# Performance work log

Measured on AMD Instinct MI355X. Metric: run time of the kernel, lower is better.

## Reference

```python
import jax, jax.numpy as jnp
import numpy as np

N_IN = 100000   # active voxels at coarse level
N_OUT = 400000  # active voxels at fine level
K = 8           # 2x2x2 kernel offsets of the inverse conv
P = 100000      # rulebook pairs per kernel offset
C_IN, C_OUT, C_SKIP = 128, 64, 64
EPS = 1e-5


def setup_inputs() -> dict:
    key = jax.random.key(0)
    k1, k2, k3, k4, k5, k6 = jax.random.split(key, 6)
    x_feats = jax.random.normal(k1, (N_IN, C_IN), jnp.float32)
    skip_feats = jax.random.normal(k2, (N_OUT, C_SKIP), jnp.float32)
    W_deconv = jax.random.normal(k3, (K, C_IN, C_OUT), jnp.float32) * (1.0 / np.sqrt(C_IN * K))
    gamma = jnp.ones((C_OUT,), jnp.float32)
    beta = jnp.zeros((C_OUT,), jnp.float32)
    W_fuse = jax.random.normal(k4, (C_OUT + C_SKIP, C_OUT), jnp.float32) * (1.0 / np.sqrt(C_OUT + C_SKIP))
    in_idx = jax.random.randint(k5, (K, P), 0, N_IN, jnp.int32)
    out_idx = jax.random.randint(k6, (K, P), 0, N_OUT, jnp.int32)
    return {"x_feats": x_feats, "skip_feats": skip_feats, "W_deconv": W_deconv,
            "gamma": gamma, "beta": beta, "W_fuse": W_fuse,
            "in_idx": in_idx, "out_idx": out_idx}


def reference(x_feats, skip_feats, W_deconv, gamma, beta, W_fuse, in_idx, out_idx):
    # --- SparseInverseConv3d: gather-GEMM-scatter over the rulebook ---
    gathered = x_feats[in_idx]                                  # [K,P,C_IN]
    contrib = jnp.einsum('kpi,kio->kpo', gathered, W_deconv)    # [K,P,C_OUT]
    y = jnp.zeros((N_OUT, C_OUT), x_feats.dtype)
    y = y.at[out_idx.reshape(-1)].add(contrib.reshape(-1, C_OUT))
    # --- BatchNorm1d (batch stats, biased var) + ReLU on voxel features ---
    mean = jnp.mean(y, axis=0)
    var = jnp.mean((y - mean) ** 2, axis=0)
    y = (y - mean) * jax.lax.rsqrt(var + EPS) * gamma + beta
    y = jax.nn.relu(y)
    # --- channel concat with skip, then SubMConv3d(kernel=1) == linear ---
    z = jnp.concatenate([y, skip_feats], axis=1)                # [N_OUT, C_OUT+C_SKIP]
    return z @ W_fuse                                           # [N_OUT, C_OUT]
```

## Files before the change

kernel.cpp:

```cpp
#include <hip/hip_runtime.h>

#define N_IN   100000
#define N_OUT  400000
#define KK     8
#define PP     100000
#define C_IN   128
#define C_OUTC 64
#define C_SKIP 64
#define EPS_BN 1e-5f
#define SLOTS  16

typedef __attribute__((ext_vector_type(8))) short bf16x8;
typedef __attribute__((ext_vector_type(4))) float f32x4;

__device__ __forceinline__ unsigned short f2b(float f) {
    unsigned int u = __builtin_bit_cast(unsigned int, f);
    return (unsigned short)((u + 0x7FFFu + ((u >> 16) & 1u)) >> 16);
}
__device__ __forceinline__ float b2f(unsigned short v) {
    return __builtin_bit_cast(float, (unsigned)v << 16);
}

__global__ __launch_bounds__(256) void prep_all(
    const float4* __restrict__ x, const float* __restrict__ Wd,
    unsigned short* __restrict__ xb, unsigned short* __restrict__ bfrag,
    int4* __restrict__ counts4)
{
    const int t = blockIdx.x * 256 + threadIdx.x;
    if (t < N_IN * C_IN / 8) {
        const float4 v0 = x[2 * t], v1 = x[2 * t + 1];
        uint4 o;
        o.x = f2b(v0.x) | ((unsigned)f2b(v0.y) << 16);
        o.y = f2b(v0.z) | ((unsigned)f2b(v0.w) << 16);
        o.z = f2b(v1.x) | ((unsigned)f2b(v1.y) << 16);
        o.w = f2b(v1.z) | ((unsigned)f2b(v1.w) << 16);
        ((uint4*)xb)[t] = o;
    }
    if (t < N_OUT / 4)
        counts4[t] = (int4){0, 0, 0, 0};
    if (t < KK * 4 * 4 * 64 * 8) {
        const int j  = t & 7;
        const int l  = (t >> 3) & 63;
        const int ct = (t >> 9) & 3;
        const int ks = (t >> 11) & 3;
        const int ko = t >> 13;
        const int i  = ks * 32 + (l >> 4) * 8 + j;
        const int c  = ct * 16 + (l & 15);
        bfrag[t] = f2b(Wd[((size_t)ko * C_IN + i) * C_OUTC + c]);
    }
}

__global__ __launch_bounds__(256) void fill_csr(
    const int* __restrict__ in_idx, const int* __restrict__ out_idx,
    int* __restrict__ counts, int* __restrict__ slots)
{
    const int q = blockIdx.x * 256 + threadIdx.x;
    if (q < KK * PP) {
        const int row = out_idx[q];
        const int pk  = in_idx[q] * KK + q / PP;
        const int idx = atomicAdd(&counts[row], 1);
        if (idx < SLOTS) slots[(size_t)row * SLOTS + idx] = pk;
    }
}

__global__ __launch_bounds__(256) void gemm_all(
    const unsigned short* __restrict__ xb, const unsigned short* __restrict__ bfrag,
    unsigned short* __restrict__ z)
{
    __shared__ __align__(16) unsigned short alds[32 * 136];
    const int rb = blockIdx.x * 32;
    for (int cch = threadIdx.x; cch < 32 * 16; cch += 256) {
        const int row = cch >> 4, ch = cch & 15;
        *(uint4*)(&alds[row * 136 + ch * 8]) =
            *(const uint4*)(xb + (size_t)(rb + row) * C_IN + ch * 8);
    }
    __syncthreads();

    const int wv  = threadIdx.x >> 6;
    const int l   = threadIdx.x & 63;
    const int r16 = l & 15, hi = l >> 4;

    f32x4 acc[2][2][4];
    #pragma unroll
    for (int q = 0; q < 2; ++q)
        #pragma unroll
        for (int rt = 0; rt < 2; ++rt)
            #pragma unroll
            for (int ct = 0; ct < 4; ++ct)
                acc[q][rt][ct] = (f32x4){0.f, 0.f, 0.f, 0.f};

    #pragma unroll
    for (int ks = 0; ks < 4; ++ks) {
        const bf16x8 a0 = *(const bf16x8*)(&alds[r16 * 136 + ks * 32 + hi * 8]);
        const bf16x8 a1 = *(const bf16x8*)(&alds[(16 + r16) * 136 + ks * 32 + hi * 8]);
        #pragma unroll
        for (int q = 0; q < 2; ++q) {
            const unsigned short* __restrict__ bk = bfrag + (size_t)(wv * 2 + q) * 8192;
            #pragma unroll
            for (int ct = 0; ct < 4; ++ct) {
                const bf16x8 b = *(const bf16x8*)(bk + ((ks * 4 + ct) * 64 + l) * 8);
                acc[q][0][ct] = __builtin_amdgcn_mfma_f32_16x16x32_bf16(a0, b, acc[q][0][ct], 0, 0, 0);
                acc[q][1][ct] = __builtin_amdgcn_mfma_f32_16x16x32_bf16(a1, b, acc[q][1][ct], 0, 0, 0);
            }
        }
    }

    #pragma unroll
    for (int q = 0; q < 2; ++q) {
        const int k = wv * 2 + q;
        #pragma unroll
        for (int rt = 0; rt < 2; ++rt)
            #pragma unroll
            for (int ct = 0; ct < 4; ++ct)
                #pragma unroll
                for (int j = 0; j < 4; ++j)
                    z[((size_t)(rb + rt * 16 + hi * 4 + j) * KK + k) * 64 + ct * 16 + r16]
                        = f2b(acc[q][rt][ct][j]);
    }
}

__global__ __launch_bounds__(256) void gather_yb(
    const unsigned short* __restrict__ z, const int* __restrict__ counts,
    const int* __restrict__ slots, unsigned short* __restrict__ yb,
    float* __restrict__ partials)
{
    const int tid = threadIdx.x, lane = tid & 63;
    const int gw  = blockIdx.x * 4 + (tid >> 6);
    const int nw  = gridDim.x * 4;
    float ssum = 0.f, ssq = 0.f;

    for (int r0 = gw * 8; r0 < N_OUT; r0 += nw * 8) {
        const int4 c0 = *(const int4*)(counts + r0);
        const int4 c1 = *(const int4*)(counts + r0 + 4);
        const int cnt[8] = {c0.x, c0.y, c0.z, c0.w, c1.x, c1.y, c1.z, c1.w};
        int4 s4[8];
        #pragma unroll
        for (int i = 0; i < 8; ++i)
            s4[i] = *(const int4*)(slots + (size_t)(r0 + i) * SLOTS);

        float a[8];
        #pragma unroll
        for (int i = 0; i < 8; ++i) {
            const int c  = cnt[i] > SLOTS ? SLOTS : cnt[i];
            const int p0 = c > 0 ? s4[i].x : 0;
            const int p1 = c > 1 ? s4[i].y : 0;
            const int p2 = c > 2 ? s4[i].z : 0;
            const int p3 = c > 3 ? s4[i].w : 0;
            const float v0 = b2f(z[(size_t)p0 * 64 + lane]);
            const float v1 = b2f(z[(size_t)p1 * 64 + lane]);
            const float v2 = b2f(z[(size_t)p2 * 64 + lane]);
            const float v3 = b2f(z[(size_t)p3 * 64 + lane]);
            float s = (c > 0 ? v0 : 0.f) + (c > 1 ? v1 : 0.f);
            s += (c > 2 ? v2 : 0.f) + (c > 3 ? v3 : 0.f);
            if (c > 4) {
                for (int j = 4; j < c; ++j)
                    s += b2f(z[(size_t)slots[(size_t)(r0 + i) * SLOTS + j] * 64 + lane]);
            }
            a[i] = s;
        }
        #pragma unroll
        for (int i = 0; i < 8; ++i) {
            yb[(size_t)(r0 + i) * C_OUTC + lane] = f2b(a[i]);
            ssum += a[i];
            ssq = fmaf(a[i], a[i], ssq);
        }
    }

    __shared__ float rs[256], rq[256];
    rs[tid] = ssum; rq[tid] = ssq;
    __syncthreads();
    if (tid < 64) {
        const float s  = rs[tid] + rs[tid + 64] + rs[tid + 128] + rs[tid + 192];
        const float q2 = rq[tid] + rq[tid + 64] + rq[tid + 128] + rq[tid + 192];
        partials[(size_t)blockIdx.x * 128 + tid]      = s;
        partials[(size_t)blockIdx.x * 128 + 64 + tid] = q2;
    }
}

__global__ __launch_bounds__(256) void gather_y(
    const unsigned short* __restrict__ z, const int* __restrict__ counts,
    const int* __restrict__ slots, float* __restrict__ y,
    float* __restrict__ partials)
{
    const int tid = threadIdx.x, lane = tid & 63;
    const int gw  = blockIdx.x * 4 + (tid >> 6);
    const int nw  = gridDim.x * 4;
    float ssum = 0.f, ssq = 0.f;

    for (int r0 = gw * 8; r0 < N_OUT; r0 += nw * 8) {
        const int4 c0 = *(const int4*)(counts + r0);
        const int4 c1 = *(const int4*)(counts + r0 + 4);
        const int cnt[8] = {c0.x, c0.y, c0.z, c0.w, c1.x, c1.y, c1.z, c1.w};
        int4 s4[8];
        #pragma unroll
        for (int i = 0; i < 8; ++i)
            s4[i] = *(const int4*)(slots + (size_t)(r0 + i) * SLOTS);

        float a[8];
        #pragma unroll
        for (int i = 0; i < 8; ++i) {
            const int c  = cnt[i] > SLOTS ? SLOTS : cnt[i];
            const int p0 = c > 0 ? s4[i].x : 0;
            const int p1 = c > 1 ? s4[i].y : 0;
            const int p2 = c > 2 ? s4[i].z : 0;
            const int p3 = c > 3 ? s4[i].w : 0;
            const float v0 = b2f(z[(size_t)p0 * 64 + lane]);
            const float v1 = b2f(z[(size_t)p1 * 64 + lane]);
            const float v2 = b2f(z[(size_t)p2 * 64 + lane]);
            const float v3 = b2f(z[(size_t)p3 * 64 + lane]);
            float s = (c > 0 ? v0 : 0.f) + (c > 1 ? v1 : 0.f);
            s += (c > 2 ? v2 : 0.f) + (c > 3 ? v3 : 0.f);
            if (c > 4) {
                for (int j = 4; j < c; ++j)
                    s += b2f(z[(size_t)slots[(size_t)(r0 + i) * SLOTS + j] * 64 + lane]);
            }
            a[i] = s;
        }
        #pragma unroll
        for (int i = 0; i < 8; ++i) {
            y[(size_t)(r0 + i) * C_OUTC + lane] = a[i];
            ssum += a[i];
            ssq = fmaf(a[i], a[i], ssq);
        }
    }

    __shared__ float rs[256], rq[256];
    rs[tid] = ssum; rq[tid] = ssq;
    __syncthreads();
    if (tid < 64) {
        const float s  = rs[tid] + rs[tid + 64] + rs[tid + 128] + rs[tid + 192];
        const float q2 = rq[tid] + rq[tid + 64] + rq[tid + 128] + rq[tid + 192];
        partials[(size_t)blockIdx.x * 128 + tid]      = s;
        partials[(size_t)blockIdx.x * 128 + 64 + tid] = q2;
    }
}

__global__ __launch_bounds__(256) void reduce_mid(
    const float* __restrict__ partials, float* __restrict__ mid)
{
    const int col = threadIdx.x & 127, half = threadIdx.x >> 7;
    const int b   = blockIdx.x;
    float s = 0.f;
    #pragma unroll 4
    for (int r = half; r < 64; r += 2)
        s += partials[(size_t)(b * 64 + r) * 128 + col];
    __shared__ float sh[256];
    sh[threadIdx.x] = s;
    __syncthreads();
    if (half == 0) mid[(size_t)b * 128 + col] = s + sh[128 + col];
}

__global__ void finalize_p(const float* __restrict__ mid,
                           const float* __restrict__ gamma,
                           const float* __restrict__ beta,
                           const float* __restrict__ Wf,
                           float* __restrict__ sc)
{
    __shared__ float acc2[128];
    __shared__ float bsh[C_OUTC];
    const int t = threadIdx.x;
    float s = 0.f;
    #pragma unroll
    for (int b = 0; b < 32; ++b) s += mid[(size_t)b * 128 + t];
    acc2[t] = s;
    __syncthreads();
    if (t < 64) {
        const float inv_n = 1.0f / (float)N_OUT;
        const float mean  = acc2[t] * inv_n;
        const float var   = acc2[64 + t] * inv_n - mean * mean;
        const float sg    = gamma[t] * rsqrtf(var + EPS_BN);
        const float b     = beta[t] - mean * sg;
        sc[t]            = sg;
        sc[C_OUTC + t]   = -b / sg;
        bsh[t] = b;
    }
    __syncthreads();
    if (t < 64) {
        float acc = 0.f;
        for (int i = 0; i < C_OUTC; ++i)
            acc = fmaf(bsh[i], Wf[i * C_OUTC + t], acc);
        sc[2 * C_OUTC + t] = acc;
    }
}

__global__ __launch_bounds__(256) void prep_ffrag(
    const float* __restrict__ Wf, const float* __restrict__ sc,
    unsigned short* __restrict__ wf_frag)
{
    const int e = blockIdx.x * 256 + threadIdx.x;
    if (e < 4 * 4 * 64 * 8) {
        const int j  = e & 7;
        const int l  = (e >> 3) & 63;
        const int ct = (e >> 9) & 3;
        const int ks = e >> 11;
        const int i  = ks * 32 + (l >> 4) * 8 + j;
        const int c  = ct * 16 + (l & 15);
        float w = Wf[(size_t)i * C_OUTC + c];
        if (i < C_OUTC) w *= sc[i];
        wf_frag[e] = f2b(w);
    }
}

__global__ __launch_bounds__(256) void fuse_mfma_b(
    const unsigned short* __restrict__ yb, const float* __restrict__ skip,
    const unsigned short* __restrict__ wf_frag, const float* __restrict__ sc,
    float* __restrict__ out)
{
    __shared__ __align__(16) unsigned short alds[128 * 136];
    __shared__ float nbsh[C_OUTC];
    const int rb = blockIdx.x * 128;
    if (threadIdx.x < C_OUTC) nbsh[threadIdx.x] = sc[C_OUTC + threadIdx.x];
    __syncthreads();

    const uint4* __restrict__ yb4 = (const uint4*)(yb + (size_t)rb * C_OUTC);
    for (int e = threadIdx.x; e < 128 * 8; e += 256) {
        const int row = e >> 3, q = e & 7;
        uint4 v = yb4[row * 8 + q];
        uint4 o;
        unsigned* vp = (unsigned*)&v;
        unsigned* op = (unsigned*)&o;
        #pragma unroll
        for (int h = 0; h < 4; ++h) {
            const float lo = fmaxf(b2f((unsigned short)(vp[h] & 0xFFFF)), nbsh[q * 8 + h * 2]);
            const float hf = fmaxf(b2f((unsigned short)(vp[h] >> 16)),    nbsh[q * 8 + h * 2 + 1]);
            op[h] = f2b(lo) | ((unsigned)f2b(hf) << 16);
        }
        *(uint4*)(&alds[row * 136 + q * 8]) = o;
    }
    const float4* __restrict__ s4 = (const float4*)(skip + (size_t)rb * C_SKIP);
    for (int e = threadIdx.x; e < 128 * 16; e += 256) {
        const int row = e >> 4, q = e & 15;
        const float4 v = s4[row * 16 + q];
        uint2 p;
        p.x = f2b(v.x) | ((unsigned)f2b(v.y) << 16);
        p.y = f2b(v.z) | ((unsigned)f2b(v.w) << 16);
        *(uint2*)(&alds[row * 136 + 64 + q * 4]) = p;
    }
    __syncthreads();

    const int w   = threadIdx.x >> 6;
    const int l   = threadIdx.x & 63;
    const int r16 = l & 15, hi = l >> 4;
    const int rw  = w * 32;

    f32x4 acc[2][4];
    #pragma unroll
    for (int ct = 0; ct < 4; ++ct) {
        const float b0 = sc[2 * C_OUTC + ct * 16 + r16];
        acc[0][ct] = (f32x4){b0, b0, b0, b0};
        acc[1][ct] = (f32x4){b0, b0, b0, b0};
    }

    #pragma unroll
    for (int ks = 0; ks < 4; ++ks) {
        const bf16x8 a0 = *(const bf16x8*)(&alds[(rw + r16) * 136 + ks * 32 + hi * 8]);
        const bf16x8 a1 = *(const bf16x8*)(&alds[(rw + 16 + r16) * 136 + ks * 32 + hi * 8]);
        #pragma unroll
        for (int ct = 0; ct < 4; ++ct) {
            const bf16x8 b = *(const bf16x8*)(wf_frag + ((ks * 4 + ct) * 64 + l) * 8);
            acc[0][ct] = __builtin_amdgcn_mfma_f32_16x16x32_bf16(a0, b, acc[0][ct], 0, 0, 0);
            acc[1][ct] = __builtin_amdgcn_mfma_f32_16x16x32_bf16(a1, b, acc[1][ct], 0, 0, 0);
        }
    }

    #pragma unroll
    for (int rt = 0; rt < 2; ++rt)
        #pragma unroll
        for (int ct = 0; ct < 4; ++ct)
            #pragma unroll
            for (int j = 0; j < 4; ++j)
                out[(size_t)(rb + rw + rt * 16 + hi * 4 + j) * C_OUTC + ct * 16 + r16]
                    = acc[rt][ct][j];
}

__global__ __launch_bounds__(256) void fuse_mfma(
    float* __restrict__ y, const float* __restrict__ skip,
    const unsigned short* __restrict__ wf_frag, const float* __restrict__ sc)
{
    __shared__ __align__(16) unsigned short alds[128 * 136];
    const int rb = blockIdx.x * 128;
    const float4* __restrict__ y4 = (const float4*)(y + (size_t)rb * C_OUTC);
    const float4* __restrict__ s4 = (const float4*)(skip + (size_t)rb * C_SKIP);
    const float4* __restrict__ nb4p = (const float4*)(sc + C_OUTC);

    for (int e = threadIdx.x; e < 128 * 32; e += 256) {
        const int row = e >> 5, q = e & 31;
        float4 v;
        if (q < 16) {
            v = y4[row * 16 + q];
            const float4 nb = nb4p[q];
            v.x = fmaxf(v.x, nb.x); v.y = fmaxf(v.y, nb.y);
            v.z = fmaxf(v.z, nb.z); v.w = fmaxf(v.w, nb.w);
        } else {
            v = s4[row * 16 + (q - 16)];
        }
        uint2 p;
        p.x = f2b(v.x) | ((unsigned)f2b(v.y) << 16);
        p.y = f2b(v.z) | ((unsigned)f2b(v.w) << 16);
        *(uint2*)(&alds[row * 136 + q * 4]) = p;
    }
    __syncthreads();

    const int w   = threadIdx.x >> 6;
    const int l   = threadIdx.x & 63;
    const int r16 = l & 15, hi = l >> 4;
    const int rw  = w * 32;

    f32x4 acc[2][4];
    #pragma unroll
    for (int ct = 0; ct < 4; ++ct) {
        const float b0 = sc[2 * C_OUTC + ct * 16 + r16];
        acc[0][ct] = (f32x4){b0, b0, b0, b0};
        acc[1][ct] = (f32x4){b0, b0, b0, b0};
    }

    #pragma unroll
    for (int ks = 0; ks < 4; ++ks) {
        const bf16x8 a0 = *(const bf16x8*)(&alds[(rw + r16) * 136 + ks * 32 + hi * 8]);
        const bf16x8 a1 = *(const bf16x8*)(&alds[(rw + 16 + r16) * 136 + ks * 32 + hi * 8]);
        #pragma unroll
        for (int ct = 0; ct < 4; ++ct) {
            const bf16x8 b = *(const bf16x8*)(wf_frag + ((ks * 4 + ct) * 64 + l) * 8);
            acc[0][ct] = __builtin_amdgcn_mfma_f32_16x16x32_bf16(a0, b, acc[0][ct], 0, 0, 0);
            acc[1][ct] = __builtin_amdgcn_mfma_f32_16x16x32_bf16(a1, b, acc[1][ct], 0, 0, 0);
        }
    }

    #pragma unroll
    for (int rt = 0; rt < 2; ++rt)
        #pragma unroll
        for (int ct = 0; ct < 4; ++ct)
            #pragma unroll
            for (int j = 0; j < 4; ++j)
                y[(size_t)(rb + rw + rt * 16 + hi * 4 + j) * C_OUTC + ct * 16 + r16]
                    = acc[rt][ct][j];
}

extern "C" void kernel_launch(void* const* d_in, const int* in_sizes, int n_in,
                              void* d_out, int out_size, void* d_ws, size_t ws_size,
                              hipStream_t stream)
{
    const float* x      = (const float*)d_in[0];
    const float* skip   = (const float*)d_in[1];
    const float* Wd     = (const float*)d_in[2];
    const float* gamma  = (const float*)d_in[3];
    const float* beta   = (const float*)d_in[4];
    const float* Wf     = (const float*)d_in[5];
    const int*   in_idx  = (const int*)d_in[6];
    const int*   out_idx = (const int*)d_in[7];

    float* y  = (float*)d_out;
    float* sc = (float*)d_ws + 128;

    char* p = (char*)d_ws + 4096;
    unsigned short* xb      = (unsigned short*)p;  p += (size_t)N_IN * C_IN * 2;
    unsigned short* bfrag   = (unsigned short*)p;  p += (size_t)KK * 8192 * 2;
    unsigned short* wf_frag = (unsigned short*)p;  p += 8192 * 2;
    int*   counts   = (int*)p;                     p += (size_t)N_OUT * 4;
    int*   slots    = (int*)p;                     p += (size_t)N_OUT * SLOTS * 4;
    float* partials = (float*)p;                   p += (size_t)2048 * 128 * 4;
    float* mid      = (float*)p;                   p += (size_t)32 * 128 * 4;
    unsigned short* z = (unsigned short*)p;        p += (size_t)N_IN * KK * C_OUTC * 2;
    unsigned short* yb = (unsigned short*)p;
    const size_t need_b = ((char*)yb - (char*)d_ws) + (size_t)N_OUT * C_OUTC * 2;
    const size_t need_f = (char*)yb - (char*)d_ws;

    prep_all<<<(N_IN * C_IN / 8 + 255) / 256, 256, 0, stream>>>(
        (const float4*)x, Wd, xb, bfrag, (int4*)counts);
    fill_csr<<<(KK * PP + 255) / 256, 256, 0, stream>>>(in_idx, out_idx, counts, slots);
    gemm_all<<<N_IN / 32, 256, 0, stream>>>(xb, bfrag, z);

    if (ws_size >= need_b) {
        gather_yb<<<2048, 256, 0, stream>>>(z, counts, slots, yb, partials);
        reduce_mid<<<32, 256, 0, stream>>>(partials, mid);
        finalize_p<<<1, 128, 0, stream>>>(mid, gamma, beta, Wf, sc);
        prep_ffrag<<<32, 256, 0, stream>>>(Wf, sc, wf_frag);
        fuse_mfma_b<<<N_OUT / 128, 256, 0, stream>>>(yb, skip, wf_frag, sc, y);
    } else if (ws_size >= need_f) {
        gather_y<<<2048, 256, 0, stream>>>(z, counts, slots, y, partials);
        reduce_mid<<<32, 256, 0, stream>>>(partials, mid);
        finalize_p<<<1, 128, 0, stream>>>(mid, gamma, beta, Wf, sc);
        prep_ffrag<<<32, 256, 0, stream>>>(Wf, sc, wf_frag);
        fuse_mfma<<<N_OUT / 128, 256, 0, stream>>>(y, skip, wf_frag, sc);
    }
}
```

Measured before the change: 267.3 us.

## Merge GEMM and CSR fill, atomic stat reduction, fold weight prep into finalize

```diff
diff --git a/kernel.cpp b/kernel.cpp
--- a/kernel.cpp
+++ b/kernel.cpp
@@ -24,7 +24,7 @@
 __global__ __launch_bounds__(256) void prep_all(
     const float4* __restrict__ x, const float* __restrict__ Wd,
     unsigned short* __restrict__ xb, unsigned short* __restrict__ bfrag,
-    int4* __restrict__ counts4)
+    int4* __restrict__ counts4, float4* __restrict__ mid4)
 {
     const int t = blockIdx.x * 256 + threadIdx.x;
     if (t < N_IN * C_IN / 8) {
@@ -38,6 +38,8 @@
     }
     if (t < N_OUT / 4)
         counts4[t] = (int4){0, 0, 0, 0};
+    if (t < (32 * 128) / 4)
+        mid4[t] = (float4){0.f, 0.f, 0.f, 0.f};
     if (t < KK * 4 * 4 * 64 * 8) {
         const int j  = t & 7;
         const int l  = (t >> 3) & 63;
@@ -50,23 +52,23 @@
     }
 }
 
-__global__ __launch_bounds__(256) void fill_csr(
+__global__ __launch_bounds__(256) void gemm_fill(
+    const unsigned short* __restrict__ xb, const unsigned short* __restrict__ bfrag,
+    unsigned short* __restrict__ z,
     const int* __restrict__ in_idx, const int* __restrict__ out_idx,
     int* __restrict__ counts, int* __restrict__ slots)
 {
-    const int q = blockIdx.x * 256 + threadIdx.x;
-    if (q < KK * PP) {
-        const int row = out_idx[q];
-        const int pk  = in_idx[q] * KK + q / PP;
-        const int idx = atomicAdd(&counts[row], 1);
-        if (idx < SLOTS) slots[(size_t)row * SLOTS + idx] = pk;
-    }
-}
-
-__global__ __launch_bounds__(256) void gemm_all(
-    const unsigned short* __restrict__ xb, const unsigned short* __restrict__ bfrag,
-    unsigned short* __restrict__ z)
-{
+    if (blockIdx.x >= N_IN / 32) {
+        const int q = ((int)blockIdx.x - N_IN / 32) * 256 + (int)threadIdx.x;
+        if (q < KK * PP) {
+            const int row = out_idx[q];
+            const int pk  = in_idx[q] * KK + q / PP;
+            const int idx = atomicAdd(&counts[row], 1);
+            if (idx < SLOTS) slots[(size_t)row * SLOTS + idx] = pk;
+        }
+        return;
+    }
+
     __shared__ __align__(16) unsigned short alds[32 * 136];
     const int rb = blockIdx.x * 32;
     for (int cch = threadIdx.x; cch < 32 * 16; cch += 256) {
@@ -119,145 +121,74 @@
     }
 }
 
-__global__ __launch_bounds__(256) void gather_yb(
+__global__ __launch_bounds__(512) void gather_yb(
     const unsigned short* __restrict__ z, const int* __restrict__ counts,
     const int* __restrict__ slots, unsigned short* __restrict__ yb,
-    float* __restrict__ partials)
+    float* __restrict__ mid)
 {
     const int tid = threadIdx.x, lane = tid & 63;
-    const int gw  = blockIdx.x * 4 + (tid >> 6);
-    const int nw  = gridDim.x * 4;
+    const int gw  = (int)blockIdx.x * 8 + (tid >> 6);
+    const int r0  = gw * 8;
+
+    const int4 c0 = *(const int4*)(counts + r0);
+    const int4 c1 = *(const int4*)(counts + r0 + 4);
+    const int cnt[8] = {c0.x, c0.y, c0.z, c0.w, c1.x, c1.y, c1.z, c1.w};
+    int4 s4[8];
+    #pragma unroll
+    for (int i = 0; i < 8; ++i)
+        s4[i] = *(const int4*)(slots + (size_t)(r0 + i) * SLOTS);
+
     float ssum = 0.f, ssq = 0.f;
-
-    for (int r0 = gw * 8; r0 < N_OUT; r0 += nw * 8) {
-        const int4 c0 = *(const int4*)(counts + r0);
-        const int4 c1 = *(const int4*)(counts + r0 + 4);
-        const int cnt[8] = {c0.x, c0.y, c0.z, c0.w, c1.x, c1.y, c1.z, c1.w};
-        int4 s4[8];
-        #pragma unroll
-        for (int i = 0; i < 8; ++i)
-            s4[i] = *(const int4*)(slots + (size_t)(r0 + i) * SLOTS);
-
-        float a[8];
-        #pragma unroll
-        for (int i = 0; i < 8; ++i) {
-            const int c  = cnt[i] > SLOTS ? SLOTS : cnt[i];
-            const int p0 = c > 0 ? s4[i].x : 0;
-            const int p1 = c > 1 ? s4[i].y : 0;
-            const int p2 = c > 2 ? s4[i].z : 0;
-            const int p3 = c > 3 ? s4[i].w : 0;
-            const float v0 = b2f(z[(size_t)p0 * 64 + lane]);
-            const float v1 = b2f(z[(size_t)p1 * 64 + lane]);
-            const float v2 = b2f(z[(size_t)p2 * 64 + lane]);
-            const float v3 = b2f(z[(size_t)p3 * 64 + lane]);
-            float s = (c > 0 ? v0 : 0.f) + (c > 1 ? v1 : 0.f);
-            s += (c > 2 ? v2 : 0.f) + (c > 3 ? v3 : 0.f);
-            if (c > 4) {
-                for (int j = 4; j < c; ++j)
-                    s += b2f(z[(size_t)slots[(size_t)(r0 + i) * SLOTS + j] * 64 + lane]);
-            }
-            a[i] = s;
-        }
-        #pragma unroll
-        for (int i = 0; i < 8; ++i) {
-            yb[(size_t)(r0 + i) * C_OUTC + lane] = f2b(a[i]);
-            ssum += a[i];
-            ssq = fmaf(a[i], a[i], ssq);
-        }
-    }
-
-    __shared__ float rs[256], rq[256];
+    float a[8];
+    #pragma unroll
+    for (int i = 0; i < 8; ++i) {
+        const int c  = cnt[i] > SLOTS ? SLOTS : cnt[i];
+        const int p0 = c > 0 ? s4[i].x : 0;
+        const int p1 = c > 1 ? s4[i].y : 0;
+        const int p2 = c > 2 ? s4[i].z : 0;
+        const int p3 = c > 3 ? s4[i].w : 0;
+        const float v0 = b2f(z[(size_t)p0 * 64 + lane]);
+        const float v1 = b2f(z[(size_t)p1 * 64 + lane]);
+        const float v2 = b2f(z[(size_t)p2 * 64 + lane]);
+        const float v3 = b2f(z[(size_t)p3 * 64 + lane]);
+        float s = (c > 0 ? v0 : 0.f) + (c > 1 ? v1 : 0.f);
+        s += (c > 2 ? v2 : 0.f) + (c > 3 ? v3 : 0.f);
+        if (c > 4) {
+            for (int j = 4; j < c; ++j)
+                s += b2f(z[(size_t)slots[(size_t)(r0 + i) * SLOTS + j] * 64 + lane]);
+        }
+        a[i] = s;
+    }
+    #pragma unroll
+    for (int i = 0; i < 8; ++i) {
+        yb[(size_t)(r0 + i) * C_OUTC + lane] = f2b(a[i]);
+        ssum += a[i];
+        ssq = fmaf(a[i], a[i], ssq);
+    }
+
+    __shared__ float rs[512], rq[512];
     rs[tid] = ssum; rq[tid] = ssq;
     __syncthreads();
     if (tid < 64) {
-        const float s  = rs[tid] + rs[tid + 64] + rs[tid + 128] + rs[tid + 192];
-        const float q2 = rq[tid] + rq[tid + 64] + rq[tid + 128] + rq[tid + 192];
-        partials[(size_t)blockIdx.x * 128 + tid]      = s;
-        partials[(size_t)blockIdx.x * 128 + 64 + tid] = q2;
-    }
-}
-
-__global__ __launch_bounds__(256) void gather_y(
-    const unsigned short* __restrict__ z, const int* __restrict__ counts,
-    const int* __restrict__ slots, float* __restrict__ y,
-    float* __restrict__ partials)
-{
-    const int tid = threadIdx.x, lane = tid & 63;
-    const int gw  = blockIdx.x * 4 + (tid >> 6);
-    const int nw  = gridDim.x * 4;
-    float ssum = 0.f, ssq = 0.f;
-
-    for (int r0 = gw * 8; r0 < N_OUT; r0 += nw * 8) {
-        const int4 c0 = *(const int4*)(counts + r0);
-        const int4 c1 = *(const int4*)(counts + r0 + 4);
-        const int cnt[8] = {c0.x, c0.y, c0.z, c0.w, c1.x, c1.y, c1.z, c1.w};
-        int4 s4[8];
-        #pragma unroll
-        for (int i = 0; i < 8; ++i)
-            s4[i] = *(const int4*)(slots + (size_t)(r0 + i) * SLOTS);
-
-        float a[8];
-        #pragma unroll
-        for (int i = 0; i < 8; ++i) {
-            const int c  = cnt[i] > SLOTS ? SLOTS : cnt[i];
-            const int p0 = c > 0 ? s4[i].x : 0;
-            const int p1 = c > 1 ? s4[i].y : 0;
-            const int p2 = c > 2 ? s4[i].z : 0;
-            const int p3 = c > 3 ? s4[i].w : 0;
-            const float v0 = b2f(z[(size_t)p0 * 64 + lane]);
-            const float v1 = b2f(z[(size_t)p1 * 64 + lane]);
-            const float v2 = b2f(z[(size_t)p2 * 64 + lane]);
-            const float v3 = b2f(z[(size_t)p3 * 64 + lane]);
-            float s = (c > 0 ? v0 : 0.f) + (c > 1 ? v1 : 0.f);
-            s += (c > 2 ? v2 : 0.f) + (c > 3 ? v3 : 0.f);
-            if (c > 4) {
-                for (int j = 4; j < c; ++j)
-                    s += b2f(z[(size_t)slots[(size_t)(r0 + i) * SLOTS + j] * 64 + lane]);
-            }
-            a[i] = s;
-        }
-        #pragma unroll
-        for (int i = 0; i < 8; ++i) {
-            y[(size_t)(r0 + i) * C_OUTC + lane] = a[i];
-            ssum += a[i];
-            ssq = fmaf(a[i], a[i], ssq);
-        }
-    }
-
-    __shared__ float rs[256], rq[256];
-    rs[tid] = ssum; rq[tid] = ssq;
-    __syncthreads();
-    if (tid < 64) {
-        const float s  = rs[tid] + rs[tid + 64] + rs[tid + 128] + rs[tid + 192];
-        const float q2 = rq[tid] + rq[tid + 64] + rq[tid + 128] + rq[tid + 192];
-        partials[(size_t)blockIdx.x * 128 + tid]      = s;
-        partials[(size_t)blockIdx.x * 128 + 64 + tid] = q2;
-    }
-}
-
-__global__ __launch_bounds__(256) void reduce_mid(
-    const float* __restrict__ partials, float* __restrict__ mid)
-{
-    const int col = threadIdx.x & 127, half = threadIdx.x >> 7;
-    const int b   = blockIdx.x;
-    float s = 0.f;
-    #pragma unroll 4
-    for (int r = half; r < 64; r += 2)
-        s += partials[(size_t)(b * 64 + r) * 128 + col];
-    __shared__ float sh[256];
-    sh[threadIdx.x] = s;
-    __syncthreads();
-    if (half == 0) mid[(size_t)b * 128 + col] = s + sh[128 + col];
+        float s = 0.f, q2 = 0.f;
+        #pragma unroll
+        for (int w = 0; w < 8; ++w) { s += rs[tid + w * 64]; q2 += rq[tid + w * 64]; }
+        float* mrow = mid + (size_t)(blockIdx.x & 31) * 128;
+        atomicAdd(&mrow[tid], s);
+        atomicAdd(&mrow[64 + tid], q2);
+    }
 }
 
 __global__ void finalize_p(const float* __restrict__ mid,
                            const float* __restrict__ gamma,
                            const float* __restrict__ beta,
                            const float* __restrict__ Wf,
-                           float* __restrict__ sc)
+                           float* __restrict__ sc,
+                           unsigned short* __restrict__ wf_frag)
 {
     __shared__ float acc2[128];
     __shared__ float bsh[C_OUTC];
+    __shared__ float ssc[C_OUTC];
     const int t = threadIdx.x;
     float s = 0.f;
     #pragma unroll
@@ -272,6 +203,7 @@
         const float b     = beta[t] - mean * sg;
         sc[t]            = sg;
         sc[C_OUTC + t]   = -b / sg;
+        ssc[t] = sg;
         bsh[t] = b;
     }
     __syncthreads();
@@ -281,14 +213,7 @@
             acc = fmaf(bsh[i], Wf[i * C_OUTC + t], acc);
         sc[2 * C_OUTC + t] = acc;
     }
-}
-
-__global__ __launch_bounds__(256) void prep_ffrag(
-    const float* __restrict__ Wf, const float* __restrict__ sc,
-    unsigned short* __restrict__ wf_frag)
-{
-    const int e = blockIdx.x * 256 + threadIdx.x;
-    if (e < 4 * 4 * 64 * 8) {
+    for (int e = t; e < 4 * 4 * 64 * 8; e += 128) {
         const int j  = e & 7;
         const int l  = (e >> 3) & 63;
         const int ct = (e >> 9) & 3;
@@ -296,7 +221,7 @@
         const int i  = ks * 32 + (l >> 4) * 8 + j;
         const int c  = ct * 16 + (l & 15);
         float w = Wf[(size_t)i * C_OUTC + c];
-        if (i < C_OUTC) w *= sc[i];
+        if (i < C_OUTC) w *= ssc[i];
         wf_frag[e] = f2b(w);
     }
 }
@@ -373,69 +298,6 @@
                     = acc[rt][ct][j];
 }
 
-__global__ __launch_bounds__(256) void fuse_mfma(
-    float* __restrict__ y, const float* __restrict__ skip,
-    const unsigned short* __restrict__ wf_frag, const float* __restrict__ sc)
-{
-    __shared__ __align__(16) unsigned short alds[128 * 136];
-    const int rb = blockIdx.x * 128;
-    const float4* __restrict__ y4 = (const float4*)(y + (size_t)rb * C_OUTC);
-    const float4* __restrict__ s4 = (const float4*)(skip + (size_t)rb * C_SKIP);
-    const float4* __restrict__ nb4p = (const float4*)(sc + C_OUTC);
-
-    for (int e = threadIdx.x; e < 128 * 32; e += 256) {
-        const int row = e >> 5, q = e & 31;
-        float4 v;
-        if (q < 16) {
-            v = y4[row * 16 + q];
-            const float4 nb = nb4p[q];
-            v.x = fmaxf(v.x, nb.x); v.y = fmaxf(v.y, nb.y);
-            v.z = fmaxf(v.z, nb.z); v.w = fmaxf(v.w, nb.w);
-        } else {
-            v = s4[row * 16 + (q - 16)];
-        }
-        uint2 p;
-        p.x = f2b(v.x) | ((unsigned)f2b(v.y) << 16);
-        p.y = f2b(v.z) | ((unsigned)f2b(v.w) << 16);
-        *(uint2*)(&alds[row * 136 + q * 4]) = p;
-    }
-    __syncthreads();
-
-    const int w   = threadIdx.x >> 6;
-    const int l   = threadIdx.x & 63;
-    const int r16 = l & 15, hi = l >> 4;
-    const int rw  = w * 32;
-
-    f32x4 acc[2][4];
-    #pragma unroll
-    for (int ct = 0; ct < 4; ++ct) {
-        const float b0 = sc[2 * C_OUTC + ct * 16 + r16];
-        acc[0][ct] = (f32x4){b0, b0, b0, b0};
-        acc[1][ct] = (f32x4){b0, b0, b0, b0};
-    }
-
-    #pragma unroll
-    for (int ks = 0; ks < 4; ++ks) {
-        const bf16x8 a0 = *(const bf16x8*)(&alds[(rw + r16) * 136 + ks * 32 + hi * 8]);
-        const bf16x8 a1 = *(const bf16x8*)(&alds[(rw + 16 + r16) * 136 + ks * 32 + hi * 8]);
-        #pragma unroll
-        for (int ct = 0; ct < 4; ++ct) {
-            const bf16x8 b = *(const bf16x8*)(wf_frag + ((ks * 4 + ct) * 64 + l) * 8);
-            acc[0][ct] = __builtin_amdgcn_mfma_f32_16x16x32_bf16(a0, b, acc[0][ct], 0, 0, 0);
-            acc[1][ct] = __builtin_amdgcn_mfma_f32_16x16x32_bf16(a1, b, acc[1][ct], 0, 0, 0);
-        }
-    }
-
-    #pragma unroll
-    for (int rt = 0; rt < 2; ++rt)
-        #pragma unroll
-        for (int ct = 0; ct < 4; ++ct)
-            #pragma unroll
-            for (int j = 0; j < 4; ++j)
-                y[(size_t)(rb + rw + rt * 16 + hi * 4 + j) * C_OUTC + ct * 16 + r16]
-                    = acc[rt][ct][j];
-}
-
 extern "C" void kernel_launch(void* const* d_in, const int* in_sizes, int n_in,
                               void* d_out, int out_size, void* d_ws, size_t ws_size,
                               hipStream_t stream)
@@ -458,29 +320,15 @@
     unsigned short* wf_frag = (unsigned short*)p;  p += 8192 * 2;
     int*   counts   = (int*)p;                     p += (size_t)N_OUT * 4;
     int*   slots    = (int*)p;                     p += (size_t)N_OUT * SLOTS * 4;
-    float* partials = (float*)p;                   p += (size_t)2048 * 128 * 4;
     float* mid      = (float*)p;                   p += (size_t)32 * 128 * 4;
     unsigned short* z = (unsigned short*)p;        p += (size_t)N_IN * KK * C_OUTC * 2;
     unsigned short* yb = (unsigned short*)p;
-    const size_t need_b = ((char*)yb - (char*)d_ws) + (size_t)N_OUT * C_OUTC * 2;
-    const size_t need_f = (char*)yb - (char*)d_ws;
 
     prep_all<<<(N_IN * C_IN / 8 + 255) / 256, 256, 0, stream>>>(
-        (const float4*)x, Wd, xb, bfrag, (int4*)counts);
-    fill_csr<<<(KK * PP + 255) / 256, 256, 0, stream>>>(in_idx, out_idx, counts, slots);
-    gemm_all<<<N_IN / 32, 256, 0, stream>>>(xb, bfrag, z);
-
-    if (ws_size >= need_b) {
-        gather_yb<<<2048, 256, 0, stream>>>(z, counts, slots, yb, partials);
-        reduce_mid<<<32, 256, 0, stream>>>(partials, mid);
-        finalize_p<<<1, 128, 0, stream>>>(mid, gamma, beta, Wf, sc);
-        prep_ffrag<<<32, 256, 0, stream>>>(Wf, sc, wf_frag);
-        fuse_mfma_b<<<N_OUT / 128, 256, 0, stream>>>(yb, skip, wf_frag, sc, y);
-    } else if (ws_size >= need_f) {
-        gather_y<<<2048, 256, 0, stream>>>(z, counts, slots, y, partials);
-        reduce_mid<<<32, 256, 0, stream>>>(partials, mid);
-        finalize_p<<<1, 128, 0, stream>>>(mid, gamma, beta, Wf, sc);
-        prep_ffrag<<<32, 256, 0, stream>>>(Wf, sc, wf_frag);
-        fuse_mfma<<<N_OUT / 128, 256, 0, stream>>>(y, skip, wf_frag, sc);
-    }
-}
+        (const float4*)x, Wd, xb, bfrag, (int4*)counts, (float4*)mid);
+    gemm_fill<<<N_IN / 32 + (KK * PP + 255) / 256, 256, 0, stream>>>(
+        xb, bfrag, z, in_idx, out_idx, counts, slots);
+    gather_yb<<<N_OUT / 64, 512, 0, stream>>>(z, counts, slots, yb, mid);
+    finalize_p<<<1, 128, 0, stream>>>(mid, gamma, beta, Wf, sc, wf_frag);
+    fuse_mfma_b<<<N_OUT / 128, 256, 0, stream>>>(yb, skip, wf_frag, sc, y);
+}
```

After: 266.6 us. No clear change (-0.3%).
